# Kernel tuning notes

Measured on AMD Instinct MI355X. Metric: run time of the kernel, lower is better.

The kernel has to match this reference:

```python
import jax, jax.numpy as jnp
import numpy as np

B, H, W, C, D = 32, 28, 28, 768, 64  # batch, height, width, input_dim, adapter dim
EMB = 64  # meta_net output / layer_embedding size


def qgelu(x):
    return x * jax.nn.sigmoid(1.702 * x)


def setup_inputs() -> dict:
    key = jax.random.key(0)
    ks = jax.random.split(key, 10)
    s = 0.02
    return {
        "x": jax.random.normal(ks[0], (B, H, W, C), jnp.float32),
        "meta_w1": jax.random.normal(ks[1], (EMB, C), jnp.float32) * s,
        "meta_b1": jnp.zeros((EMB,), jnp.float32),
        "meta_w2": jax.random.normal(ks[2], (EMB, EMB), jnp.float32) * s,
        "meta_b2": jnp.zeros((EMB,), jnp.float32),
        "layer_emb": jax.random.normal(ks[3], (EMB,), jnp.float32),
        "hyper_w": jax.random.normal(ks[4], (D * D * 9, EMB), jnp.float32) * s,
        "hyper_b": jnp.zeros((D * D * 9,), jnp.float32),
        "down_w": jax.random.normal(ks[5], (D, C), jnp.float32) * np.sqrt(6.0 / (C + D)),
        "down_b": jnp.zeros((D,), jnp.float32),
        "up_w": jax.random.normal(ks[6], (C, D), jnp.float32) * s,  # torch inits zeros; random for nontrivial test
        "up_b": jnp.zeros((C,), jnp.float32),
    }


def reference(x, meta_w1, meta_b1, meta_w2, meta_b2, layer_emb,
              hyper_w, hyper_b, down_w, down_b, up_w, up_b):
    # meta_net: Linear -> ReLU -> Linear, then mean over (H, W)
    h = jax.nn.relu(jnp.einsum('bhwc,oc->bhwo', x, meta_w1) + meta_b1)
    prompt = (jnp.einsum('bhwo,po->bhwp', h, meta_w2) + meta_b2).mean(axis=(1, 2))  # [B, EMB]
    # fuse_type == 'add'
    fused = layer_emb[None, :] + prompt  # [B, EMB]
    # hypernet -> per-sample conv weights [B, D, D, 3, 3]
    conv_w = (fused @ hyper_w.T + hyper_b).reshape(-1, D, D, 3, 3)
    # adapter_down + QuickGELU
    x_down = jnp.einsum('bhwc,dc->bhwd', x, down_w) + down_b  # [B,H,W,D]
    x_patch = qgelu(x_down).transpose(0, 3, 1, 2)  # [B,D,H,W]
    # per-sample 3x3 conv, stride 1, padding 1 (vmapped over batch)
    def conv1(xi, wi):
        return jax.lax.conv_general_dilated(xi[None], wi, (1, 1), [(1, 1), (1, 1)])[0]
    y = jax.vmap(conv1)(x_patch, conv_w)  # [B,D,H,W]
    y = qgelu(y.transpose(0, 2, 3, 1))  # [B,H,W,D]; dropout is identity in eval
    return jnp.einsum('bhwd,cd->bhwc', y, up_w) + up_b
```

## Files before the change

### kernel.cpp

```cpp
#include <hip/hip_runtime.h>
#include <math.h>

#define B_    32
#define H_    28
#define W_    28
#define C_    768
#define D_    64
#define EMB_  64
#define HW_   (H_ * W_)
#define NPOS  (B_ * HW_)
#define CWROWS (D_ * D_ * 9)

typedef __attribute__((ext_vector_type(8))) short bf16x8;
typedef __attribute__((ext_vector_type(4))) float f32x4;

__device__ __forceinline__ float qgelu(float v) {
    return v / (1.f + __expf(-1.702f * v));
}
__device__ __forceinline__ float relu(float v) { return fmaxf(v, 0.f); }

__device__ __forceinline__ ushort f2bf(float f) {
    union { float f; unsigned u; } v; v.f = f;
    return (ushort)((v.u + 0x7fffu + ((v.u >> 16) & 1u)) >> 16);
}

__device__ __forceinline__ void* swz(void* base, int row, int kbyte) {
    return (void*)((char*)base + row * 128 + (kbyte ^ ((row & 7) << 4)));
}

__global__ void k_cvt(const float* __restrict__ w1, const float* __restrict__ dw,
                      const float* __restrict__ uw,
                      ushort* __restrict__ wcat, ushort* __restrict__ wup)
{
    const int f = (blockIdx.x * 256 + threadIdx.x) * 4;
    const float* src;
    ushort* dst;
    if (f < 49152)      { src = w1 + f;           dst = wcat + f; }
    else if (f < 98304) { src = dw + (f - 49152); dst = wcat + f; }
    else                { src = uw + (f - 98304); dst = wup + (f - 98304); }
    float4 v = *(const float4*)src;
    union { ushort u[4]; uint2 p; } o;
    o.u[0] = f2bf(v.x); o.u[1] = f2bf(v.y); o.u[2] = f2bf(v.z); o.u[3] = f2bf(v.w);
    *(uint2*)dst = o.p;
}

__global__ __launch_bounds__(512)
void k_gemm_md(const float* __restrict__ x, const ushort* __restrict__ wcat,
               const float* __restrict__ b1, const float* __restrict__ db,
               float* __restrict__ hbuf, ushort* __restrict__ xact)
{
    __shared__ ushort As[64 * 64];
    __shared__ ushort Bs[128 * 64];
    const int t = threadIdx.x;
    const int wid = t >> 6, lane = t & 63;
    const int lo = lane & 15, hi = lane >> 4;
    const int bm = blockIdx.x;

    f32x4 acc[4] = {};

    const int arow = t >> 3, akseg = t & 7;
    const float* asrc = x + (size_t)(bm * 64 + arow) * C_ + akseg * 8;

    for (int k0 = 0; k0 < C_; k0 += 64) {
        __syncthreads();
        {
            float4 v0 = *(const float4*)(asrc + k0);
            float4 v1 = *(const float4*)(asrc + k0 + 4);
            union { ushort u[8]; float4 v; } tmp;
            tmp.u[0] = f2bf(v0.x); tmp.u[1] = f2bf(v0.y);
            tmp.u[2] = f2bf(v0.z); tmp.u[3] = f2bf(v0.w);
            tmp.u[4] = f2bf(v1.x); tmp.u[5] = f2bf(v1.y);
            tmp.u[6] = f2bf(v1.z); tmp.u[7] = f2bf(v1.w);
            *(float4*)swz(As, arow, akseg * 16) = tmp.v;
        }
        #pragma unroll
        for (int s = 0; s < 2; ++s) {
            int j = s * 512 + t;
            int n = j >> 3, kseg = j & 7;
            *(float4*)swz(Bs, n, kseg * 16) =
                *(const float4*)(wcat + (size_t)n * C_ + k0 + kseg * 8);
        }
        __syncthreads();
        #pragma unroll
        for (int ks = 0; ks < 2; ++ks) {
            bf16x8 b = *(const bf16x8*)swz(Bs, wid * 16 + lo, ks * 64 + hi * 16);
            #pragma unroll
            for (int i = 0; i < 4; ++i) {
                bf16x8 a = *(const bf16x8*)swz(As, i * 16 + lo, ks * 64 + hi * 16);
                acc[i] = __builtin_amdgcn_mfma_f32_16x16x32_bf16(a, b, acc[i], 0, 0, 0);
            }
        }
    }

    const int n = wid * 16 + lo;
    if (wid < 4) {
        const float bias = b1[n];
        #pragma unroll
        for (int i = 0; i < 4; ++i)
            #pragma unroll
            for (int r = 0; r < 4; ++r) {
                int pos = bm * 64 + i * 16 + hi * 4 + r;
                hbuf[(size_t)pos * 64 + n] = relu(acc[i][r] + bias);
            }
    } else {
        const float bias = db[n - 64];
        #pragma unroll
        for (int i = 0; i < 4; ++i)
            #pragma unroll
            for (int r = 0; r < 4; ++r) {
                int pos = bm * 64 + i * 16 + hi * 4 + r;
                xact[(size_t)pos * 64 + (n - 64)] = f2bf(qgelu(acc[i][r] + bias));
            }
    }
}

__global__ void k_reduce1(const float* __restrict__ hbuf, float* __restrict__ partial)
{
    __shared__ float part[16][EMB_];
    const int b = blockIdx.x, q = blockIdx.y;
    const int tid = threadIdx.x;
    const int e4 = tid & 15, pc = tid >> 4;

    const float* base = hbuf + ((size_t)b * HW_ + q * 196) * 64 + e4 * 4;
    float4 acc = make_float4(0.f, 0.f, 0.f, 0.f);
    for (int i = pc; i < 196; i += 16) {
        float4 v = *(const float4*)(base + (size_t)i * 64);
        acc.x += v.x; acc.y += v.y; acc.z += v.z; acc.w += v.w;
    }
    part[pc][e4 * 4 + 0] = acc.x;
    part[pc][e4 * 4 + 1] = acc.y;
    part[pc][e4 * 4 + 2] = acc.z;
    part[pc][e4 * 4 + 3] = acc.w;
    __syncthreads();
    if (tid < EMB_) {
        float s = 0.f;
        #pragma unroll
        for (int c = 0; c < 16; ++c) s += part[c][tid];
        partial[(size_t)(b * 4 + q) * EMB_ + tid] = s;
    }
}

__global__ void k_reduce2(const float* __restrict__ partial,
                          const float* __restrict__ w2, const float* __restrict__ b2,
                          float* __restrict__ prompt)
{
    __shared__ float hm[EMB_];
    const int b = blockIdx.x;
    const int e = threadIdx.x;
    float s = partial[(size_t)(b * 4 + 0) * EMB_ + e]
            + partial[(size_t)(b * 4 + 1) * EMB_ + e]
            + partial[(size_t)(b * 4 + 2) * EMB_ + e]
            + partial[(size_t)(b * 4 + 3) * EMB_ + e];
    hm[e] = s * (1.f / HW_);
    __syncthreads();
    const float4* w2r = (const float4*)(w2 + (size_t)e * EMB_);
    const float4* hm4 = (const float4*)hm;
    float a0 = 0.f, a1 = 0.f, a2 = 0.f, a3 = 0.f;
    #pragma unroll
    for (int i = 0; i < EMB_ / 4; ++i) {
        float4 h = hm4[i], w = w2r[i];
        a0 = fmaf(h.x, w.x, a0); a1 = fmaf(h.y, w.y, a1);
        a2 = fmaf(h.z, w.z, a2); a3 = fmaf(h.w, w.w, a3);
    }
    prompt[b * EMB_ + e] = (a0 + a1) + (a2 + a3) + b2[e];
}

__global__ void k_hyper(const float* __restrict__ prompt, const float* __restrict__ layer_emb,
                        const float* __restrict__ hyper_w, const float* __restrict__ hyper_b,
                        ushort* __restrict__ cwb)
{
    __shared__ float fused[B_][EMB_];
    const int tid = threadIdx.x;
    for (int i = tid; i < B_ * EMB_; i += 256) {
        int e = i & (EMB_ - 1);
        fused[i >> 6][e] = layer_emb[e] + prompt[i];
    }
    __syncthreads();

    const int f    = blockIdx.x * 256 + tid;
    const int din  = f & 63;
    const int dout = (f >> 6) & 63;
    const int tap  = f >> 12;
    const int r    = (dout * 64 + din) * 9 + tap;

    float wrow[EMB_];
    const float4* hw4 = (const float4*)(hyper_w + (size_t)r * EMB_);
    #pragma unroll
    for (int i = 0; i < EMB_ / 4; ++i) {
        float4 v = hw4[i];
        wrow[i*4+0] = v.x; wrow[i*4+1] = v.y; wrow[i*4+2] = v.z; wrow[i*4+3] = v.w;
    }
    const float hb = hyper_b[r];

    const int b0 = blockIdx.y * 8;
    for (int b = b0; b < b0 + 8; ++b) {
        float a0 = 0.f, a1 = 0.f, a2 = 0.f, a3 = 0.f;
        #pragma unroll
        for (int i = 0; i < EMB_; i += 4) {
            a0 = fmaf(fused[b][i+0], wrow[i+0], a0);
            a1 = fmaf(fused[b][i+1], wrow[i+1], a1);
            a2 = fmaf(fused[b][i+2], wrow[i+2], a2);
            a3 = fmaf(fused[b][i+3], wrow[i+3], a3);
        }
        cwb[(size_t)b * CWROWS + f] = f2bf((a0 + a1) + (a2 + a3) + hb);
    }
}

__global__ __launch_bounds__(512)
void k_conv(const ushort* __restrict__ xact, const ushort* __restrict__ cwb,
            ushort* __restrict__ yact)
{
    __shared__ ushort wsl[192 * 64];
    __shared__ ushort xs[34 * 64];
    const int t = threadIdx.x;
    const int lane = t & 63;
    const int lo = lane & 15, hi = lane >> 4;
    const int b = blockIdx.x / H_;
    const int h = blockIdx.x % H_;
    const int mtile = (t >> 6) >> 2;
    const int ntile = (t >> 6) & 3;
    const int w0 = mtile * 16;

    f32x4 acc = {};

    for (int kh = 0; kh < 3; ++kh) {
        const int hh = h + kh - 1;
        __syncthreads();
        const ushort* wsrc = cwb + (size_t)b * CWROWS + (size_t)kh * 3 * 4096;
        #pragma unroll
        for (int s = 0; s < 3; ++s) {
            int j = s * 512 + t;
            *(float4*)swz(wsl, j >> 3, (j & 7) * 16) = *(const float4*)(wsrc + j * 8);
        }
        if (t < 272) {
            int c = t >> 3, kseg = t & 7;
            int w = c - 1;
            float4 v = make_float4(0.f, 0.f, 0.f, 0.f);
            if (hh >= 0 && hh < H_ && w >= 0 && w < W_)
                v = *(const float4*)(xact + ((size_t)((b * H_ + hh) * W_) + w) * 64 + kseg * 8);
            *(float4*)swz(xs, c, kseg * 16) = v;
        }
        __syncthreads();
        #pragma unroll
        for (int kw = 0; kw < 3; ++kw) {
            #pragma unroll
            for (int ks = 0; ks < 2; ++ks) {
                bf16x8 a  = *(const bf16x8*)swz(xs, w0 + lo + kw, ks * 64 + hi * 16);
                bf16x8 bf = *(const bf16x8*)swz(wsl, kw * 64 + ntile * 16 + lo, ks * 64 + hi * 16);
                acc = __builtin_amdgcn_mfma_f32_16x16x32_bf16(a, bf, acc, 0, 0, 0);
            }
        }
    }

    const int dout = ntile * 16 + lo;
    #pragma unroll
    for (int r = 0; r < 4; ++r) {
        int w = w0 + hi * 4 + r;
        if (w < W_)
            yact[((size_t)((b * H_ + h) * W_) + w) * 64 + dout] = f2bf(qgelu(acc[r]));
    }
}

__global__ __launch_bounds__(512)
void k_up(const ushort* __restrict__ yact, const ushort* __restrict__ wup,
          const float* __restrict__ ub, float* __restrict__ out)
{
    __shared__ ushort As[64 * 64];
    __shared__ ushort Bs[256 * 64];
    const int t = threadIdx.x;
    const int wid = t >> 6, lane = t & 63;
    const int lo = lane & 15, hi = lane >> 4;
    const int bm = blockIdx.x;

    {
        int row = t >> 3, kseg = t & 7;
        *(float4*)swz(As, row, kseg * 16) =
            *(const float4*)(yact + (size_t)(bm * 64 + row) * 64 + kseg * 8);
    }

    for (int nc = 0; nc < 3; ++nc) {
        __syncthreads();
        #pragma unroll
        for (int s = 0; s < 4; ++s) {
            int j = s * 512 + t;
            int n = j >> 3, kseg = j & 7;
            *(float4*)swz(Bs, n, kseg * 16) =
                *(const float4*)(wup + (size_t)(nc * 256 + n) * 64 + kseg * 8);
        }
        __syncthreads();

        f32x4 acc[4][2] = {};
        #pragma unroll
        for (int ks = 0; ks < 2; ++ks) {
            bf16x8 a[4], b[2];
            #pragma unroll
            for (int i = 0; i < 4; ++i)
                a[i] = *(const bf16x8*)swz(As, i * 16 + lo, ks * 64 + hi * 16);
            #pragma unroll
            for (int j = 0; j < 2; ++j)
                b[j] = *(const bf16x8*)swz(Bs, wid * 32 + j * 16 + lo, ks * 64 + hi * 16);
            #pragma unroll
            for (int i = 0; i < 4; ++i)
                #pragma unroll
                for (int j = 0; j < 2; ++j)
                    acc[i][j] = __builtin_amdgcn_mfma_f32_16x16x32_bf16(a[i], b[j], acc[i][j], 0, 0, 0);
        }

        #pragma unroll
        for (int j = 0; j < 2; ++j) {
            const int n = nc * 256 + wid * 32 + j * 16 + lo;
            const float bias = ub[n];
            #pragma unroll
            for (int i = 0; i < 4; ++i)
                #pragma unroll
                for (int r = 0; r < 4; ++r) {
                    int pos = bm * 64 + i * 16 + hi * 4 + r;
                    out[(size_t)pos * C_ + n] = acc[i][j][r] + bias;
                }
        }
    }
}

extern "C" void kernel_launch(void* const* d_in, const int* in_sizes, int n_in,
                              void* d_out, int out_size, void* d_ws, size_t ws_size,
                              hipStream_t stream) {
    const float* x         = (const float*)d_in[0];
    const float* meta_w1   = (const float*)d_in[1];
    const float* meta_b1   = (const float*)d_in[2];
    const float* meta_w2   = (const float*)d_in[3];
    const float* meta_b2   = (const float*)d_in[4];
    const float* layer_emb = (const float*)d_in[5];
    const float* hyper_w   = (const float*)d_in[6];
    const float* hyper_b   = (const float*)d_in[7];
    const float* down_w    = (const float*)d_in[8];
    const float* down_b    = (const float*)d_in[9];
    const float* up_w      = (const float*)d_in[10];
    const float* up_b      = (const float*)d_in[11];
    float* out = (float*)d_out;

    char* p = (char*)d_ws;
    float*  hbuf    = (float*)p;           p += (size_t)NPOS * 64 * 4;
    ushort* yact    = (ushort*)hbuf;
    ushort* xact    = (ushort*)p;          p += (size_t)NPOS * 64 * 2;
    float*  prompt  = (float*)p;           p += (size_t)B_ * EMB_ * 4;
    float*  partial = (float*)p;           p += (size_t)B_ * 4 * EMB_ * 4;
    ushort* cwb     = (ushort*)p;          p += (size_t)B_ * CWROWS * 2;
    ushort* wcat    = (ushort*)p;          p += (size_t)128 * C_ * 2;
    ushort* wup     = (ushort*)p;

    k_cvt<<<144, 256, 0, stream>>>(meta_w1, down_w, up_w, wcat, wup);
    k_gemm_md<<<NPOS / 64, 512, 0, stream>>>(x, wcat, meta_b1, down_b, hbuf, xact);
    k_reduce1<<<dim3(B_, 4), 256, 0, stream>>>(hbuf, partial);
    k_reduce2<<<B_, 64, 0, stream>>>(partial, meta_w2, meta_b2, prompt);
    dim3 hgrid(CWROWS / 256, B_ / 8);
    k_hyper<<<hgrid, 256, 0, stream>>>(prompt, layer_emb, hyper_w, hyper_b, cwb);
    k_conv<<<B_ * H_, 512, 0, stream>>>(xact, cwb, yact);
    k_up<<<NPOS / 64, 512, 0, stream>>>(yact, wup, up_b, out);
}
```

Measured before the change: 69.72 us.

## Pre-swizzle bf16 weights and stage them into LDS via direct global_load_lds

The weight-conversion kernel now writes meta_w1/down_w and up_w in a pre-swizzled, k-blocked layout. The GEMM kernels can then copy weight tiles straight into LDS with global_load_lds and skip the register round trip. The down/meta GEMM also prefetches the next x tile into registers across the barrier and switches to a 2x2 warp tiling so A and B fragments are reused. This is meant to cut VGPR traffic and load latency during LDS staging. In exchange it ties correctness to the swizzle matching between the writer and reader.

```diff
diff --git a/kernel.cpp b/kernel.cpp
--- a/kernel.cpp
+++ b/kernel.cpp
@@ -28,24 +28,41 @@
     return (void*)((char*)base + row * 128 + (kbyte ^ ((row & 7) << 4)));
 }
 
+typedef const __attribute__((address_space(1))) void g_void;
+typedef __attribute__((address_space(3))) void l_void;
+__device__ __forceinline__ void gload16(const void* g, void* l) {
+    __builtin_amdgcn_global_load_lds((g_void*)g, (l_void*)l, 16, 0, 0);
+}
+
 __global__ void k_cvt(const float* __restrict__ w1, const float* __restrict__ dw,
                       const float* __restrict__ uw,
-                      ushort* __restrict__ wcat, ushort* __restrict__ wup)
+                      ushort* __restrict__ wcat2, ushort* __restrict__ wup2)
 {
     const int f = (blockIdx.x * 256 + threadIdx.x) * 4;
-    const float* src;
-    ushort* dst;
-    if (f < 49152)      { src = w1 + f;           dst = wcat + f; }
-    else if (f < 98304) { src = dw + (f - 49152); dst = wcat + f; }
-    else                { src = uw + (f - 98304); dst = wup + (f - 98304); }
-    float4 v = *(const float4*)src;
+    float4 v;
+    size_t dst;
+    ushort* base;
+    if (f < 98304) {
+        int n, k;
+        if (f < 49152) { n = f / 768;            k = f % 768; v = *(const float4*)(w1 + (size_t)n * 768 + k); }
+        else           { int g = f - 49152; n = 64 + g / 768; k = g % 768; v = *(const float4*)(dw + (size_t)(n - 64) * 768 + k); }
+        const int kb = k >> 6, kk = k & 63;
+        dst  = (size_t)kb * 8192 + n * 64 + (kk ^ ((n & 7) << 3));
+        base = wcat2;
+    } else {
+        const int g = f - 98304;
+        const int n = g >> 6, kk = g & 63;
+        v = *(const float4*)(uw + g);
+        dst  = (size_t)n * 64 + (kk ^ ((n & 7) << 3));
+        base = wup2;
+    }
     union { ushort u[4]; uint2 p; } o;
     o.u[0] = f2bf(v.x); o.u[1] = f2bf(v.y); o.u[2] = f2bf(v.z); o.u[3] = f2bf(v.w);
-    *(uint2*)dst = o.p;
+    *(uint2*)(base + dst) = o.p;
 }
 
 __global__ __launch_bounds__(512)
-void k_gemm_md(const float* __restrict__ x, const ushort* __restrict__ wcat,
+void k_gemm_md(const float* __restrict__ x, const ushort* __restrict__ wcat2,
                const float* __restrict__ b1, const float* __restrict__ db,
                float* __restrict__ hbuf, ushort* __restrict__ xact)
 {
@@ -54,63 +71,80 @@
     const int t = threadIdx.x;
     const int wid = t >> 6, lane = t & 63;
     const int lo = lane & 15, hi = lane >> 4;
+    const int mw = wid >> 2, nw = wid & 3;
     const int bm = blockIdx.x;
 
-    f32x4 acc[4] = {};
-
-    const int arow = t >> 3, akseg = t & 7;
-    const float* asrc = x + (size_t)(bm * 64 + arow) * C_ + akseg * 8;
+    f32x4 acc[2][2] = {};
+
+    const int arow = t >> 3, akq = t & 7;
+    const float* asrc = x + (size_t)(bm * 64 + arow) * C_ + akq * 8;
+
+    float4 p0 = *(const float4*)(asrc);
+    float4 p1 = *(const float4*)(asrc + 4);
 
     for (int k0 = 0; k0 < C_; k0 += 64) {
         __syncthreads();
         {
-            float4 v0 = *(const float4*)(asrc + k0);
-            float4 v1 = *(const float4*)(asrc + k0 + 4);
             union { ushort u[8]; float4 v; } tmp;
-            tmp.u[0] = f2bf(v0.x); tmp.u[1] = f2bf(v0.y);
-            tmp.u[2] = f2bf(v0.z); tmp.u[3] = f2bf(v0.w);
-            tmp.u[4] = f2bf(v1.x); tmp.u[5] = f2bf(v1.y);
-            tmp.u[6] = f2bf(v1.z); tmp.u[7] = f2bf(v1.w);
-            *(float4*)swz(As, arow, akseg * 16) = tmp.v;
-        }
-        #pragma unroll
-        for (int s = 0; s < 2; ++s) {
-            int j = s * 512 + t;
-            int n = j >> 3, kseg = j & 7;
-            *(float4*)swz(Bs, n, kseg * 16) =
-                *(const float4*)(wcat + (size_t)n * C_ + k0 + kseg * 8);
-        }
-        __syncthreads();
+            tmp.u[0] = f2bf(p0.x); tmp.u[1] = f2bf(p0.y);
+            tmp.u[2] = f2bf(p0.z); tmp.u[3] = f2bf(p0.w);
+            tmp.u[4] = f2bf(p1.x); tmp.u[5] = f2bf(p1.y);
+            tmp.u[6] = f2bf(p1.z); tmp.u[7] = f2bf(p1.w);
+            *(float4*)swz(As, arow, akq * 16) = tmp.v;
+        }
+        {
+            const ushort* bsrc = wcat2 + (size_t)(k0 >> 6) * 8192;
+            #pragma unroll
+            for (int c = 0; c < 2; ++c) {
+                const int cbase = (wid * 2 + c) * 512;
+                gload16(bsrc + cbase + lane * 8, (ushort*)Bs + cbase);
+            }
+        }
+        if (k0 + 64 < C_) {
+            p0 = *(const float4*)(asrc + k0 + 64);
+            p1 = *(const float4*)(asrc + k0 + 68);
+        }
+        __syncthreads();
+
         #pragma unroll
         for (int ks = 0; ks < 2; ++ks) {
-            bf16x8 b = *(const bf16x8*)swz(Bs, wid * 16 + lo, ks * 64 + hi * 16);
-            #pragma unroll
-            for (int i = 0; i < 4; ++i) {
-                bf16x8 a = *(const bf16x8*)swz(As, i * 16 + lo, ks * 64 + hi * 16);
-                acc[i] = __builtin_amdgcn_mfma_f32_16x16x32_bf16(a, b, acc[i], 0, 0, 0);
-            }
-        }
-    }
-
-    const int n = wid * 16 + lo;
-    if (wid < 4) {
-        const float bias = b1[n];
-        #pragma unroll
-        for (int i = 0; i < 4; ++i)
-            #pragma unroll
-            for (int r = 0; r < 4; ++r) {
-                int pos = bm * 64 + i * 16 + hi * 4 + r;
-                hbuf[(size_t)pos * 64 + n] = relu(acc[i][r] + bias);
-            }
-    } else {
-        const float bias = db[n - 64];
-        #pragma unroll
-        for (int i = 0; i < 4; ++i)
-            #pragma unroll
-            for (int r = 0; r < 4; ++r) {
-                int pos = bm * 64 + i * 16 + hi * 4 + r;
-                xact[(size_t)pos * 64 + (n - 64)] = f2bf(qgelu(acc[i][r] + bias));
-            }
+            bf16x8 a[2], b[2];
+            #pragma unroll
+            for (int i = 0; i < 2; ++i)
+                a[i] = *(const bf16x8*)swz(As, mw * 32 + i * 16 + lo, ks * 64 + hi * 16);
+            #pragma unroll
+            for (int j = 0; j < 2; ++j)
+                b[j] = *(const bf16x8*)swz(Bs, nw * 32 + j * 16 + lo, ks * 64 + hi * 16);
+            #pragma unroll
+            for (int i = 0; i < 2; ++i)
+                #pragma unroll
+                for (int j = 0; j < 2; ++j)
+                    acc[i][j] = __builtin_amdgcn_mfma_f32_16x16x32_bf16(a[i], b[j], acc[i][j], 0, 0, 0);
+        }
+    }
+
+    #pragma unroll
+    for (int j = 0; j < 2; ++j) {
+        const int n = nw * 32 + j * 16 + lo;
+        if (n < 64) {
+            const float bias = b1[n];
+            #pragma unroll
+            for (int i = 0; i < 2; ++i)
+                #pragma unroll
+                for (int r = 0; r < 4; ++r) {
+                    int pos = bm * 64 + mw * 32 + i * 16 + hi * 4 + r;
+                    hbuf[(size_t)pos * 64 + n] = relu(acc[i][j][r] + bias);
+                }
+        } else {
+            const float bias = db[n - 64];
+            #pragma unroll
+            for (int i = 0; i < 2; ++i)
+                #pragma unroll
+                for (int r = 0; r < 4; ++r) {
+                    int pos = bm * 64 + mw * 32 + i * 16 + hi * 4 + r;
+                    xact[(size_t)pos * 64 + (n - 64)] = f2bf(qgelu(acc[i][j][r] + bias));
+                }
+        }
     }
 }
 
@@ -262,7 +296,7 @@
 }
 
 __global__ __launch_bounds__(512)
-void k_up(const ushort* __restrict__ yact, const ushort* __restrict__ wup,
+void k_up(const ushort* __restrict__ yact, const ushort* __restrict__ wup2,
           const float* __restrict__ ub, float* __restrict__ out)
 {
     __shared__ ushort As[64 * 64];
@@ -280,12 +314,13 @@
 
     for (int nc = 0; nc < 3; ++nc) {
         __syncthreads();
-        #pragma unroll
-        for (int s = 0; s < 4; ++s) {
-            int j = s * 512 + t;
-            int n = j >> 3, kseg = j & 7;
-            *(float4*)swz(Bs, n, kseg * 16) =
-                *(const float4*)(wup + (size_t)(nc * 256 + n) * 64 + kseg * 8);
+        {
+            const ushort* bsrc = wup2 + (size_t)nc * 16384;
+            #pragma unroll
+            for (int c = 0; c < 4; ++c) {
+                const int cbase = (wid * 4 + c) * 512;
+                gload16(bsrc + cbase + lane * 8, (ushort*)Bs + cbase);
+            }
         }
         __syncthreads();
 
@@ -345,15 +380,15 @@
     float*  prompt  = (float*)p;           p += (size_t)B_ * EMB_ * 4;
     float*  partial = (float*)p;           p += (size_t)B_ * 4 * EMB_ * 4;
     ushort* cwb     = (ushort*)p;          p += (size_t)B_ * CWROWS * 2;
-    ushort* wcat    = (ushort*)p;          p += (size_t)128 * C_ * 2;
-    ushort* wup     = (ushort*)p;
-
-    k_cvt<<<144, 256, 0, stream>>>(meta_w1, down_w, up_w, wcat, wup);
-    k_gemm_md<<<NPOS / 64, 512, 0, stream>>>(x, wcat, meta_b1, down_b, hbuf, xact);
+    ushort* wcat2   = (ushort*)p;          p += (size_t)128 * C_ * 2;
+    ushort* wup2    = (ushort*)p;
+
+    k_cvt<<<144, 256, 0, stream>>>(meta_w1, down_w, up_w, wcat2, wup2);
+    k_gemm_md<<<NPOS / 64, 512, 0, stream>>>(x, wcat2, meta_b1, down_b, hbuf, xact);
     k_reduce1<<<dim3(B_, 4), 256, 0, stream>>>(hbuf, partial);
     k_reduce2<<<B_, 64, 0, stream>>>(partial, meta_w2, meta_b2, prompt);
     dim3 hgrid(CWROWS / 256, B_ / 8);
     k_hyper<<<hgrid, 256, 0, stream>>>(prompt, layer_emb, hyper_w, hyper_b, cwb);
     k_conv<<<B_ * H_, 512, 0, stream>>>(xact, cwb, yact);
-    k_up<<<NPOS / 64, 512, 0, stream>>>(yact, wup, up_b, out);
-}
+    k_up<<<NPOS / 64, 512, 0, stream>>>(yact, wup2, up_b, out);
+}
```

Result: slower. 72.45 us (+3.9%).
